# Kernel optimization log

Hardware: AMD Instinct MI355X
Metric: run time of the kernel (lower is better)

Reference implementation:

```python
import jax, jax.numpy as jnp
import numpy as np

B, S, D, H = 4, 2048, 1024, 16
HD = D // H  # head dim = 64


def setup_inputs() -> dict:
    key = jax.random.key(0)
    ks = jax.random.split(key, 5)
    scale = 1.0 / np.sqrt(D)
    return {
        "X": jax.random.normal(ks[0], (B, S, D), dtype=jnp.float32),
        "Wq": jax.random.normal(ks[1], (D, D), dtype=jnp.float32) * scale,
        "Wk": jax.random.normal(ks[2], (D, D), dtype=jnp.float32) * scale,
        "Wv": jax.random.normal(ks[3], (D, D), dtype=jnp.float32) * scale,
        "Wo": jax.random.normal(ks[4], (D, D), dtype=jnp.float32) * scale,
    }


def _split_heads(x):
    # [B, S, D] -> [B, H, S, HD]
    b, s, d = x.shape
    return x.reshape(b, s, H, HD).transpose(0, 2, 1, 3)


def reference(X, Wq, Wk, Wv, Wo):
    q = _split_heads(X @ Wq)  # [B, H, S, HD]
    k = _split_heads(X @ Wk)
    v = _split_heads(X @ Wv)
    scores = jnp.einsum("bhqd,bhkd->bhqk", q, k) / jnp.sqrt(jnp.float32(HD))
    causal = jnp.tril(jnp.ones((S, S), dtype=bool))  # [S, S]
    scores = jnp.where(causal[None, None, :, :], scores, jnp.float32(-jnp.inf))
    attn = jax.nn.softmax(scores, axis=-1)
    out = jnp.einsum("bhqk,bhkd->bhqd", attn, v)  # [B, H, S, HD]
    out = out.transpose(0, 2, 1, 3).reshape(B, S, D)  # merge heads
    return out @ Wo
```

## Files before the change

### kernel.cpp

```cpp
#include <hip/hip_runtime.h>
#include <hip/hip_bf16.h>

typedef __attribute__((ext_vector_type(8))) short short8;
typedef __attribute__((ext_vector_type(8))) unsigned short ushort8;
typedef __attribute__((ext_vector_type(4))) unsigned short bf16x4;
typedef __attribute__((ext_vector_type(4))) float f32x4;

#define BDIM 1024
#define SEQ  2048
#define NHD  16
#define NEGBIG (-1.0e30f)

__device__ __forceinline__ unsigned short f2bf(float x) {
  union { __hip_bfloat16 h; unsigned short u; } cv;
  cv.h = __float2bfloat16(x);
  return cv.u;
}

__device__ __forceinline__ void gload16(const void* g, void* l) {
  __builtin_amdgcn_global_load_lds((const __attribute__((address_space(1))) void*)g,
                                   (__attribute__((address_space(3))) void*)l, 16, 0, 0);
}

__global__ __launch_bounds__(256) void cvt_f32_bf16(const float* __restrict__ src,
                                                    unsigned short* __restrict__ dst) {
  int i = (blockIdx.x * 256 + threadIdx.x) * 8;
  float4 a = *(const float4*)(src + i);
  float4 b = *(const float4*)(src + i + 4);
  ushort8 o;
  o[0] = f2bf(a.x); o[1] = f2bf(a.y); o[2] = f2bf(a.z); o[3] = f2bf(a.w);
  o[4] = f2bf(b.x); o[5] = f2bf(b.y); o[6] = f2bf(b.z); o[7] = f2bf(b.w);
  *(ushort8*)(dst + i) = o;
}

__global__ __launch_bounds__(256) void wtrans(const float* __restrict__ src,
                                              unsigned short* __restrict__ dst) {
  __shared__ float t[32][33];
  int tx = threadIdx.x, ty = threadIdx.y;
  int c0 = blockIdx.x * 32, r0 = blockIdx.y * 32;
  for (int i = ty; i < 32; i += 8)
    t[i][tx] = src[(size_t)(r0 + i) * BDIM + c0 + tx];
  __syncthreads();
  for (int i = ty; i < 32; i += 8)
    dst[(size_t)(c0 + i) * BDIM + r0 + tx] = f2bf(t[tx][i]);
}

template <bool F32OUT>
__global__ __launch_bounds__(256) void gemm_bt(const unsigned short* __restrict__ A,
                                               const unsigned short* __restrict__ BT,
                                               void* __restrict__ Cv) {
  __shared__ __align__(16) unsigned short As[128 * 64];
  __shared__ __align__(16) unsigned short Bs[128 * 64];
  const int tid = threadIdx.x;
  const int lane = tid & 63;
  const int w = tid >> 6;
  const int wr = w >> 1, wc = w & 1;
  const int m0 = blockIdx.x * 128;
  const int n0 = blockIdx.y * 128;
  const int l15 = lane & 15, lg = lane >> 4;

  f32x4 acc[4][4] = {};

  for (int k0 = 0; k0 < BDIM; k0 += 64) {
    for (int j = 0; j < 4; ++j) {
      int ob = (w * 4 + j) * 1024;
      int o = ob + lane * 16;
      int row = o >> 7;
      int kb = (o & 127) ^ ((row & 7) << 4);
      gload16(A + (size_t)(m0 + row) * BDIM + k0 + (kb >> 1), (char*)As + ob);
      gload16(BT + (size_t)(n0 + row) * BDIM + k0 + (kb >> 1), (char*)Bs + ob);
    }
    __syncthreads();
    for (int ks = 0; ks < 64; ks += 32) {
      int kb = (ks + lg * 8) * 2;
      short8 a[4], b[4];
      for (int mi = 0; mi < 4; ++mi) {
        int row = wr * 64 + mi * 16 + l15;
        a[mi] = *(const short8*)((const char*)As + row * 128 + (kb ^ ((row & 7) << 4)));
      }
      for (int nj = 0; nj < 4; ++nj) {
        int row = wc * 64 + nj * 16 + l15;
        b[nj] = *(const short8*)((const char*)Bs + row * 128 + (kb ^ ((row & 7) << 4)));
      }
      for (int mi = 0; mi < 4; ++mi)
        for (int nj = 0; nj < 4; ++nj)
          acc[mi][nj] = __builtin_amdgcn_mfma_f32_16x16x32_bf16(a[mi], b[nj], acc[mi][nj], 0, 0, 0);
    }
    __syncthreads();
  }
  for (int mi = 0; mi < 4; ++mi)
    for (int nj = 0; nj < 4; ++nj) {
      int m = m0 + wr * 64 + mi * 16 + lg * 4;
      int n = n0 + wc * 64 + nj * 16 + l15;
      for (int r = 0; r < 4; ++r) {
        if constexpr (F32OUT)
          ((float*)Cv)[(size_t)(m + r) * BDIM + n] = acc[mi][nj][r];
        else
          ((unsigned short*)Cv)[(size_t)(m + r) * BDIM + n] = f2bf(acc[mi][nj][r]);
      }
    }
}

__global__ __launch_bounds__(256) void attn(const unsigned short* __restrict__ Qg,
                                            const unsigned short* __restrict__ Kg,
                                            const unsigned short* __restrict__ Vg,
                                            unsigned short* __restrict__ Og) {
  __shared__ __align__(16) unsigned short Sbuf[16384];
  unsigned short* Ks  = Sbuf;
  unsigned short* VTs = Sbuf + 4096;
  unsigned short* Ps  = Sbuf + 8192;

  const int tid = threadIdx.x;
  const int lane = tid & 63;
  const int w = tid >> 6;
  const int l15 = lane & 15, lg = lane >> 4;
  const int bh = blockIdx.y;
  const size_t base = ((size_t)(bh >> 4) * SEQ) * BDIM + (size_t)(bh & 15) * 64;
  constexpr float C = 0.125f * 1.44269504089f;

  for (int half = 0; half < 2; ++half) {
    const int qt = half == 0 ? (int)blockIdx.x : 15 - (int)blockIdx.x;
    const int q0 = qt * 128;

    for (int j = 0; j < 4; ++j) {
      int o = (w * 4 + j) * 1024 + lane * 16;
      int row = o >> 7;
      int kb = o & 127;
      ushort8 qv = *(const ushort8*)(Qg + base + (size_t)(q0 + row) * BDIM + (kb >> 1));
      *(ushort8*)((char*)Sbuf + row * 128 + (kb ^ ((row & 7) << 4))) = qv;
    }
    __syncthreads();
    short8 qf[2][2];
    for (int mi = 0; mi < 2; ++mi)
      for (int ks = 0; ks < 2; ++ks) {
        int row = w * 32 + mi * 16 + l15;
        int kb = ks * 64 + lg * 16;
        qf[mi][ks] = *(const short8*)((const char*)Sbuf + row * 128 + (kb ^ ((row & 7) << 4)));
      }
    __syncthreads();

    float mrow[2] = {NEGBIG, NEGBIG}, lrow[2] = {0.f, 0.f};
    f32x4 oacc[2][4] = {};

    const int ntiles = qt * 2 + 2;
    for (int t = 0; t < ntiles; ++t) {
      const int kv0 = t * 64;
      for (int j = 0; j < 2; ++j) {
        int o = (w * 2 + j) * 1024 + lane * 16;
        int row = o >> 7;
        int kb = o & 127;
        ushort8 kv8 = *(const ushort8*)(Kg + base + (size_t)(kv0 + row) * BDIM + (kb >> 1));
        *(ushort8*)((char*)Ks + row * 128 + (kb ^ ((row & 7) << 4))) = kv8;
      }
      {
        int p = tid >> 3, dc8 = tid & 7;
        const unsigned short* vs = Vg + base + (size_t)(kv0 + 2 * p) * BDIM + dc8 * 8;
        ushort8 v0 = *(const ushort8*)vs;
        ushort8 v1 = *(const ushort8*)(vs + BDIM);
        for (int e = 0; e < 8; ++e) {
          int d = dc8 * 8 + e;
          unsigned int pk = (unsigned int)v0[e] | ((unsigned int)v1[e] << 16);
          *(unsigned int*)((char*)VTs + d * 128 + ((4 * p) ^ ((((d & 7) ^ (d >> 3)) & 7) << 4))) = pk;
        }
      }
      __syncthreads();

      if (kv0 <= q0 + w * 32 + 31) {
        f32x4 s2[2][4];
        for (int kvj = 0; kvj < 4; ++kvj) {
          int row = kvj * 16 + l15;
          int sz = (row & 7) << 4;
          short8 kf0 = *(const short8*)((const char*)Ks + row * 128 + ((lg * 16) ^ sz));
          short8 kf1 = *(const short8*)((const char*)Ks + row * 128 + ((64 + lg * 16) ^ sz));
          for (int mi = 0; mi < 2; ++mi) {
            f32x4 z = {};
            z = __builtin_amdgcn_mfma_f32_16x16x32_bf16(kf0, qf[mi][0], z, 0, 0, 0);
            z = __builtin_amdgcn_mfma_f32_16x16x32_bf16(kf1, qf[mi][1], z, 0, 0, 0);
            s2[mi][kvj] = z;
          }
        }
        for (int mi = 0; mi < 2; ++mi) {
          const int qbase = q0 + w * 32 + mi * 16;
          const int qc = qbase + l15;
          float mx = NEGBIG;
          if (kv0 + 63 > qbase) {
            for (int kvj = 0; kvj < 4; ++kvj)
              for (int r = 0; r < 4; ++r) {
                int kv = kv0 + kvj * 16 + 4 * lg + r;
                float v = s2[mi][kvj][r];
                if (kv > qc) { v = NEGBIG; s2[mi][kvj][r] = v; }
                mx = fmaxf(mx, v);
              }
          } else {
            for (int kvj = 0; kvj < 4; ++kvj)
              for (int r = 0; r < 4; ++r) mx = fmaxf(mx, s2[mi][kvj][r]);
          }
          mx = fmaxf(mx, __shfl_xor(mx, 16));
          mx = fmaxf(mx, __shfl_xor(mx, 32));
          if (!__all(mx <= mrow[mi])) {
            float mnew = fmaxf(mrow[mi], mx);
            float sc = __builtin_amdgcn_exp2f((mrow[mi] - mnew) * C);
            mrow[mi] = mnew;
            lrow[mi] *= sc;
            for (int di = 0; di < 4; ++di)
              for (int r = 0; r < 4; ++r) oacc[mi][di][r] *= sc;
          }
          const float mC = mrow[mi] * C;
          float rs = 0.f;
          for (int kvj = 0; kvj < 4; ++kvj)
            for (int r = 0; r < 4; ++r) {
              float p = __builtin_amdgcn_exp2f(fmaf(s2[mi][kvj][r], C, -mC));
              s2[mi][kvj][r] = p;
              rs += p;
            }
          rs += __shfl_xor(rs, 16);
          rs += __shfl_xor(rs, 32);
          lrow[mi] += rs;
          int prow = w * 32 + mi * 16 + l15;
          int psz = (prow & 7) << 4;
          for (int kvj = 0; kvj < 4; ++kvj) {
            bf16x4 pk;
            pk[0] = f2bf(s2[mi][kvj][0]); pk[1] = f2bf(s2[mi][kvj][1]);
            pk[2] = f2bf(s2[mi][kvj][2]); pk[3] = f2bf(s2[mi][kvj][3]);
            *(bf16x4*)((char*)Ps + prow * 128 + ((kvj * 32 + lg * 8) ^ psz)) = pk;
          }
        }
        for (int ks = 0; ks < 2; ++ks) {
          short8 pa[2], vf[4];
          for (int mi = 0; mi < 2; ++mi) {
            int row = w * 32 + mi * 16 + l15;
            pa[mi] = *(const short8*)((const char*)Ps + row * 128 +
                                      ((ks * 64 + lg * 16) ^ ((row & 7) << 4)));
          }
          for (int di = 0; di < 4; ++di) {
            int d = di * 16 + l15;
            vf[di] = *(const short8*)((const char*)VTs + d * 128 +
                                      ((ks * 64 + lg * 16) ^ ((((d & 7) ^ (d >> 3)) & 7) << 4)));
          }
          for (int mi = 0; mi < 2; ++mi)
            for (int di = 0; di < 4; ++di)
              oacc[mi][di] = __builtin_amdgcn_mfma_f32_16x16x32_bf16(vf[di], pa[mi], oacc[mi][di], 0, 0, 0);
        }
      }
      __syncthreads();
    }

    for (int mi = 0; mi < 2; ++mi) {
      float inv = 1.0f / lrow[mi];
      int qrow = q0 + w * 32 + mi * 16 + l15;
      for (int di = 0; di < 4; ++di) {
        bf16x4 ov;
        for (int r = 0; r < 4; ++r) ov[r] = f2bf(oacc[mi][di][r] * inv);
        *(bf16x4*)(Og + base + (size_t)qrow * BDIM + di * 16 + 4 * lg) = ov;
      }
    }
  }
}

extern "C" void kernel_launch(void* const* d_in, const int* in_sizes, int n_in,
                              void* d_out, int out_size, void* d_ws, size_t ws_size,
                              hipStream_t stream) {
  const float* X  = (const float*)d_in[0];
  const float* Wq = (const float*)d_in[1];
  const float* Wk = (const float*)d_in[2];
  const float* Wv = (const float*)d_in[3];
  const float* Wo = (const float*)d_in[4];

  const size_t WSZ = (size_t)1024 * 1024;
  const size_t MSZ = (size_t)8192 * 1024;
  const size_t need = (4 * WSZ + 4 * MSZ) * 2;
  if (ws_size < need) return;

  unsigned short* ws = (unsigned short*)d_ws;
  unsigned short* WqT = ws;
  unsigned short* WkT = WqT + WSZ;
  unsigned short* WvT = WkT + WSZ;
  unsigned short* WoT = WvT + WSZ;
  unsigned short* Qw  = WoT + WSZ;
  unsigned short* Kw  = Qw + MSZ;
  unsigned short* Vw  = Kw + MSZ;
  unsigned short* Ow  = Vw + MSZ;
  unsigned short* Xb  = (unsigned short*)d_out;

  dim3 tb(32, 8);
  dim3 tg(32, 32);
  wtrans<<<tg, tb, 0, stream>>>(Wq, WqT);
  wtrans<<<tg, tb, 0, stream>>>(Wk, WkT);
  wtrans<<<tg, tb, 0, stream>>>(Wv, WvT);
  wtrans<<<tg, tb, 0, stream>>>(Wo, WoT);

  cvt_f32_bf16<<<(8192 * 1024) / (256 * 8), 256, 0, stream>>>(X, Xb);

  dim3 gg(64, 8);
  gemm_bt<false><<<gg, 256, 0, stream>>>(Xb, WqT, Qw);
  gemm_bt<false><<<gg, 256, 0, stream>>>(Xb, WkT, Kw);
  gemm_bt<false><<<gg, 256, 0, stream>>>(Xb, WvT, Vw);

  attn<<<dim3(8, 64), 256, 0, stream>>>(Qw, Kw, Vw, Ow);

  gemm_bt<true><<<gg, 256, 0, stream>>>(Ow, WoT, d_out);
}
```

Measured before the change: 204.6 us.

## Enlarge attention query tile to 256 rows with 512-thread blocks

The attention kernel now uses 8 waves per block covering 256 query rows. Each K/V tile loaded into shared memory is therefore reused by twice as many query rows, and the grid shrinks to 64x4 with causal load balancing done by pairing chunk c with chunk 7-c. The K and V staging loads are redistributed across the 512 threads, and the P buffer grows. The aim is to halve K/V global traffic and staging overhead, at the cost of fewer blocks, more LDS per block, and more causal-mask waste per tile.

```diff
diff --git a/kernel.cpp b/kernel.cpp
--- a/kernel.cpp
+++ b/kernel.cpp
@@ -101,33 +101,32 @@
     }
 }
 
-__global__ __launch_bounds__(256) void attn(const unsigned short* __restrict__ Qg,
+__global__ __launch_bounds__(512) void attn(const unsigned short* __restrict__ Qg,
                                             const unsigned short* __restrict__ Kg,
                                             const unsigned short* __restrict__ Vg,
                                             unsigned short* __restrict__ Og) {
-  __shared__ __align__(16) unsigned short Sbuf[16384];
-  unsigned short* Ks  = Sbuf;
-  unsigned short* VTs = Sbuf + 4096;
-  unsigned short* Ps  = Sbuf + 8192;
+  __shared__ __align__(16) unsigned short Ks[64 * 64];
+  __shared__ __align__(16) unsigned short VTs[64 * 64];
+  __shared__ __align__(16) unsigned short Ps[256 * 64];
 
   const int tid = threadIdx.x;
   const int lane = tid & 63;
   const int w = tid >> 6;
   const int l15 = lane & 15, lg = lane >> 4;
-  const int bh = blockIdx.y;
+  const int bh = blockIdx.x;
   const size_t base = ((size_t)(bh >> 4) * SEQ) * BDIM + (size_t)(bh & 15) * 64;
   constexpr float C = 0.125f * 1.44269504089f;
 
   for (int half = 0; half < 2; ++half) {
-    const int qt = half == 0 ? (int)blockIdx.x : 15 - (int)blockIdx.x;
-    const int q0 = qt * 128;
+    const int c = half == 0 ? (int)blockIdx.y : 7 - (int)blockIdx.y;
+    const int q0 = c * 256;
 
     for (int j = 0; j < 4; ++j) {
-      int o = (w * 4 + j) * 1024 + lane * 16;
+      int o = (j * 512 + tid) * 16;
       int row = o >> 7;
       int kb = o & 127;
       ushort8 qv = *(const ushort8*)(Qg + base + (size_t)(q0 + row) * BDIM + (kb >> 1));
-      *(ushort8*)((char*)Sbuf + row * 128 + (kb ^ ((row & 7) << 4))) = qv;
+      *(ushort8*)((char*)Ps + row * 128 + (kb ^ ((row & 7) << 4))) = qv;
     }
     __syncthreads();
     short8 qf[2][2];
@@ -135,32 +134,32 @@
       for (int ks = 0; ks < 2; ++ks) {
         int row = w * 32 + mi * 16 + l15;
         int kb = ks * 64 + lg * 16;
-        qf[mi][ks] = *(const short8*)((const char*)Sbuf + row * 128 + (kb ^ ((row & 7) << 4)));
+        qf[mi][ks] = *(const short8*)((const char*)Ps + row * 128 + (kb ^ ((row & 7) << 4)));
       }
     __syncthreads();
 
     float mrow[2] = {NEGBIG, NEGBIG}, lrow[2] = {0.f, 0.f};
     f32x4 oacc[2][4] = {};
 
-    const int ntiles = qt * 2 + 2;
+    const int ntiles = 4 * c + 4;
     for (int t = 0; t < ntiles; ++t) {
       const int kv0 = t * 64;
-      for (int j = 0; j < 2; ++j) {
-        int o = (w * 2 + j) * 1024 + lane * 16;
+      {
+        int o = tid * 16;
         int row = o >> 7;
         int kb = o & 127;
         ushort8 kv8 = *(const ushort8*)(Kg + base + (size_t)(kv0 + row) * BDIM + (kb >> 1));
         *(ushort8*)((char*)Ks + row * 128 + (kb ^ ((row & 7) << 4))) = kv8;
       }
       {
-        int p = tid >> 3, dc8 = tid & 7;
-        const unsigned short* vs = Vg + base + (size_t)(kv0 + 2 * p) * BDIM + dc8 * 8;
-        ushort8 v0 = *(const ushort8*)vs;
-        ushort8 v1 = *(const ushort8*)(vs + BDIM);
-        for (int e = 0; e < 8; ++e) {
-          int d = dc8 * 8 + e;
+        int vp = tid & 31, vd = tid >> 5;
+        const unsigned short* vs = Vg + base + (size_t)(kv0 + 2 * vp) * BDIM + vd * 4;
+        bf16x4 v0 = *(const bf16x4*)vs;
+        bf16x4 v1 = *(const bf16x4*)(vs + BDIM);
+        for (int e = 0; e < 4; ++e) {
+          int d = vd * 4 + e;
           unsigned int pk = (unsigned int)v0[e] | ((unsigned int)v1[e] << 16);
-          *(unsigned int*)((char*)VTs + d * 128 + ((4 * p) ^ ((((d & 7) ^ (d >> 3)) & 7) << 4))) = pk;
+          *(unsigned int*)((char*)VTs + d * 128 + ((4 * vp) ^ ((((d & 7) ^ (d >> 3)) & 7) << 4))) = pk;
         }
       }
       __syncthreads();
@@ -296,7 +295,7 @@
   gemm_bt<false><<<gg, 256, 0, stream>>>(Xb, WkT, Kw);
   gemm_bt<false><<<gg, 256, 0, stream>>>(Xb, WvT, Vw);
 
-  attn<<<dim3(8, 64), 256, 0, stream>>>(Qw, Kw, Vw, Ow);
+  attn<<<dim3(64, 4), 512, 0, stream>>>(Qw, Kw, Vw, Ow);
 
   gemm_bt<true><<<gg, 256, 0, stream>>>(Ow, WoT, d_out);
 }
```

Result: slower. 209.8 us (+2.5%).
